# Optimization experiments

Measured on AMD Instinct MI355X. Metric: run time of the kernel, lower is better.

## Reference

```python
import jax, jax.numpy as jnp
import numpy as np


def setup_inputs() -> dict:
    key = jax.random.key(0)
    encoded_feature = jax.random.normal(key, (32, 28, 28, 512), dtype=jnp.float32)
    return {"encoded_feature": encoded_feature}


def reference(encoded_feature) -> jnp.ndarray:
    # Original op: filter = square(encoded_feature[0]) with shape [H,W,C,1],
    # input = 0/1 box mask of shape [B,2H,2W,C] (ones in the centered HxW box),
    # out = conv2d(mask, filter, VALID) -> [B, H+1, W+1, 1].
    # Since the mask is a 0/1 box identical across batch and channels,
    # out[b,i,j] = sum of square(x[0]) (summed over C) over the window of
    # filter taps that land inside the box. We compute this exactly via a
    # 2D integral image instead of a full-extent convolution.
    x = encoded_feature
    B, H, W, C = x.shape
    fsq = jnp.sum(jnp.square(x[0]), axis=-1)  # [H, W], channel-summed squared filter

    # Integral image I[r, c] = sum(fsq[:r, :c]); shape [H+1, W+1]
    I = jnp.pad(jnp.cumsum(jnp.cumsum(fsq, axis=0), axis=1), ((1, 0), (1, 0)))

    # For output position (i, j), filter tap (di, dj) overlaps the box iff
    # H/2 <= i+di < H/2 + H  and  W/2 <= j+dj < W/2 + W.
    i = jnp.arange(H + 1)
    j = jnp.arange(W + 1)
    r0 = jnp.clip(H // 2 - i, 0, H)          # window row start (inclusive)
    r1 = jnp.clip(H // 2 + H - i, 0, H)      # window row end (exclusive)
    c0 = jnp.clip(W // 2 - j, 0, W)
    c1 = jnp.clip(W // 2 + W - j, 0, W)

    out2d = (I[r1[:, None], c1[None, :]] - I[r0[:, None], c1[None, :]]
             - I[r1[:, None], c0[None, :]] + I[r0[:, None], c0[None, :]])  # [H+1, W+1]

    # Identical for every batch element (mask is batch-constant)
    return jnp.broadcast_to(out2d[None, :, :, None], (B, H + 1, W + 1, 1))
```

## Files before the change

### kernel.cpp

```cpp
#include <hip/hip_runtime.h>
#include <hip/hip_bf16.h>


#define HH 28
#define WW 28
#define CC 512
#define BB 32
#define OUTHW ((HH + 1) * (WW + 1))

__global__ void __launch_bounds__(128)
fsq_kernel(const float* __restrict__ x, float* __restrict__ fsq) {
    const int hw = blockIdx.x;
    const float4* p = reinterpret_cast<const float4*>(x + (size_t)hw * CC);
    const int t = threadIdx.x;
    float4 v = p[t];
    float s = v.x * v.x + v.y * v.y + v.z * v.z + v.w * v.w;
    #pragma unroll
    for (int off = 32; off > 0; off >>= 1)
        s += __shfl_down(s, off, 64);
    __shared__ float partial[2];
    if ((t & 63) == 0) partial[t >> 6] = s;
    __syncthreads();
    if (t == 0) fsq[hw] = partial[0] + partial[1];
}

__global__ void __launch_bounds__(256)
box_kernel(const float* __restrict__ fsq, float* __restrict__ out) {
    __shared__ float I[HH + 1][WW + 2];
    __shared__ float o2[OUTHW];
    const int t = threadIdx.x;

    if (t < WW + 1) I[0][t] = 0.f;
    if (t < HH + 1) I[t][0] = 0.f;
    for (int idx = t; idx < HH * WW; idx += 256) {
        int r = idx / WW, c = idx % WW;
        I[r + 1][c + 1] = fsq[idx];
    }
    __syncthreads();

    if (t < HH) {
        float s = 0.f;
        #pragma unroll
        for (int c = 1; c <= WW; ++c) { s += I[t + 1][c]; I[t + 1][c] = s; }
    }
    __syncthreads();

    if (t < WW) {
        float s = 0.f;
        #pragma unroll
        for (int r = 1; r <= HH; ++r) { s += I[r][t + 1]; I[r][t + 1] = s; }
    }
    __syncthreads();

    for (int idx = t; idx < OUTHW; idx += 256) {
        int i = idx / (WW + 1), j = idx % (WW + 1);
        int r0 = min(max(HH / 2 - i, 0), HH);
        int r1 = min(max(HH / 2 + HH - i, 0), HH);
        int c0 = min(max(WW / 2 - j, 0), WW);
        int c1 = min(max(WW / 2 + WW - j, 0), WW);
        o2[idx] = I[r1][c1] - I[r0][c1] - I[r1][c0] + I[r0][c0];
    }
    __syncthreads();

    for (int idx = t; idx < BB * OUTHW; idx += 256) {
        out[idx] = o2[idx % OUTHW];
    }
}

extern "C" void kernel_launch(void* const* d_in, const int* in_sizes, int n_in,
                              void* d_out, int out_size, void* d_ws, size_t ws_size,
                              hipStream_t stream) {
    const float* x = (const float*)d_in[0];
    float* out = (float*)d_out;
    float* fsq = (float*)d_ws;

    fsq_kernel<<<HH * WW, 128, 0, stream>>>(x, fsq);
    box_kernel<<<1, 256, 0, stream>>>(fsq, out);
}
```

Baseline: 83.16 us.

## Fuse reduction and box-sum kernels via last-block atomic counter

```diff
diff --git a/kernel.cpp b/kernel.cpp
--- a/kernel.cpp
+++ b/kernel.cpp
@@ -6,54 +6,62 @@
 #define WW 28
 #define CC 512
 #define BB 32
-#define OUTHW ((HH + 1) * (WW + 1))
+#define NHW (HH * WW)
+#define OH (HH + 1)
+#define OW (WW + 1)
+#define OUTHW (OH * OW)
 
-__global__ void __launch_bounds__(128)
-fsq_kernel(const float* __restrict__ x, float* __restrict__ fsq) {
+__global__ void __launch_bounds__(256)
+fused_bsq_kernel(const float* __restrict__ x, float* __restrict__ out,
+                 float* __restrict__ fsq, unsigned int* __restrict__ counter) {
     const int hw = blockIdx.x;
-    const float4* p = reinterpret_cast<const float4*>(x + (size_t)hw * CC);
-    const int t = threadIdx.x;
-    float4 v = p[t];
-    float s = v.x * v.x + v.y * v.y + v.z * v.z + v.w * v.w;
+    const int t  = threadIdx.x;
+
+    float2 v = reinterpret_cast<const float2*>(x + (size_t)hw * CC)[t];
+    float s = v.x * v.x + v.y * v.y;
     #pragma unroll
     for (int off = 32; off > 0; off >>= 1)
         s += __shfl_down(s, off, 64);
-    __shared__ float partial[2];
-    if ((t & 63) == 0) partial[t >> 6] = s;
+    __shared__ float part[4];
+    __shared__ int lastFlag;
+    if ((t & 63) == 0) part[t >> 6] = s;
     __syncthreads();
-    if (t == 0) fsq[hw] = partial[0] + partial[1];
-}
+    if (t == 0) {
+        fsq[hw] = part[0] + part[1] + part[2] + part[3];
+        __threadfence();
+        unsigned r = atomicAdd(counter, 1u);
+        lastFlag = (r == NHW - 1) ? 1 : 0;
+    }
+    __syncthreads();
+    if (!lastFlag) return;
+    __threadfence();
 
-__global__ void __launch_bounds__(256)
-box_kernel(const float* __restrict__ fsq, float* __restrict__ out) {
-    __shared__ float I[HH + 1][WW + 2];
-    __shared__ float o2[OUTHW];
-    const int t = threadIdx.x;
-
-    if (t < WW + 1) I[0][t] = 0.f;
-    if (t < HH + 1) I[t][0] = 0.f;
-    for (int idx = t; idx < HH * WW; idx += 256) {
+    __shared__ float I[OH][WW + 2];
+    if (t < OW) I[0][t] = 0.f;
+    if (t < OH) I[t][0] = 0.f;
+    for (int idx = t; idx < NHW; idx += 256) {
         int r = idx / WW, c = idx % WW;
         I[r + 1][c + 1] = fsq[idx];
     }
     __syncthreads();
 
     if (t < HH) {
-        float s = 0.f;
+        float s2 = 0.f;
         #pragma unroll
-        for (int c = 1; c <= WW; ++c) { s += I[t + 1][c]; I[t + 1][c] = s; }
+        for (int c = 1; c <= WW; ++c) { s2 += I[t + 1][c]; I[t + 1][c] = s2; }
     }
     __syncthreads();
 
     if (t < WW) {
-        float s = 0.f;
+        float s2 = 0.f;
         #pragma unroll
-        for (int r = 1; r <= HH; ++r) { s += I[r][t + 1]; I[r][t + 1] = s; }
+        for (int r = 1; r <= HH; ++r) { s2 += I[r][t + 1]; I[r][t + 1] = s2; }
     }
     __syncthreads();
 
+    __shared__ float o2[OUTHW];
     for (int idx = t; idx < OUTHW; idx += 256) {
-        int i = idx / (WW + 1), j = idx % (WW + 1);
+        int i = idx / OW, j = idx % OW;
         int r0 = min(max(HH / 2 - i, 0), HH);
         int r1 = min(max(HH / 2 + HH - i, 0), HH);
         int c0 = min(max(WW / 2 - j, 0), WW);
@@ -62,9 +70,8 @@
     }
     __syncthreads();
 
-    for (int idx = t; idx < BB * OUTHW; idx += 256) {
+    for (int idx = t; idx < BB * OUTHW; idx += 256)
         out[idx] = o2[idx % OUTHW];
-    }
 }
 
 extern "C" void kernel_launch(void* const* d_in, const int* in_sizes, int n_in,
@@ -73,7 +80,8 @@
     const float* x = (const float*)d_in[0];
     float* out = (float*)d_out;
     float* fsq = (float*)d_ws;
+    unsigned int* counter = (unsigned int*)((char*)d_ws + 4096);
 
-    fsq_kernel<<<HH * WW, 128, 0, stream>>>(x, fsq);
-    box_kernel<<<1, 256, 0, stream>>>(fsq, out);
+    hipMemsetAsync(counter, 0, sizeof(unsigned int), stream);
+    fused_bsq_kernel<<<NHW, 256, 0, stream>>>(x, out, fsq, counter);
 }
```

Result: slower. 99.69 us (+19.9%).
